# Performance work log

Hardware: AMD Instinct MI355X
Metric: run time of the kernel (lower is better)

## Reference

```python
import jax, jax.numpy as jnp
import numpy as np

B, S, E, H = 2, 2048, 2048, 16
D = E // H

def setup_inputs() -> dict:
    key = jax.random.key(0)
    ks = jax.random.split(key, 9)
    sc = 1.0 / np.sqrt(E)
    return {
        "x":  jax.random.normal(ks[0], (B, S, E), jnp.float32),
        "Wq": jax.random.normal(ks[1], (E, E), jnp.float32) * sc,
        "bq": jax.random.normal(ks[2], (E,), jnp.float32) * 0.01,
        "Wk": jax.random.normal(ks[3], (E, E), jnp.float32) * sc,
        "bk": jax.random.normal(ks[4], (E,), jnp.float32) * 0.01,
        "Wv": jax.random.normal(ks[5], (E, E), jnp.float32) * sc,
        "bv": jax.random.normal(ks[6], (E,), jnp.float32) * 0.01,
        "Wo": jax.random.normal(ks[7], (E, E), jnp.float32) * sc,
        "bo": jax.random.normal(ks[8], (E,), jnp.float32) * 0.01,
    }

def _split_heads(t):
    # [B,S,E] -> [B,H,S,D]
    return t.reshape(B, S, H, D).transpose(0, 2, 1, 3)

def reference(x, Wq, bq, Wk, bk, Wv, bv, Wo, bo):
    # projections (nn.Linear: y = x @ W^T + b)
    q = _split_heads(x @ Wq.T + bq)
    k = _split_heads(x @ Wk.T + bk)
    v = _split_heads(x @ Wv.T + bv)

    # scaled causal attention; scale uses k.size(-1) == head_dim D
    scores = jnp.einsum("bhqd,bhkd->bhqk", q, k) / jnp.sqrt(jnp.asarray(D, q.dtype))
    causal = jnp.tril(jnp.ones((S, S), bool))  # [S,S]
    scores = jnp.where(causal[None, None, :, :], scores, -jnp.inf)
    # training path subtracts row max before softmax (no-op under stable softmax)
    scores = scores - jnp.max(scores, axis=-1, keepdims=True)
    attn = jax.nn.softmax(scores, axis=-1)
    # dropout_rate = 0.0 -> identity
    ctx = jnp.einsum("bhqk,bhkd->bhqd", attn, v)

    # merge heads [B,H,S,D] -> [B,S,E], final projection
    out = ctx.transpose(0, 2, 1, 3).reshape(B, S, E)
    return out @ Wo.T + bo
```

## Files before the change

### kernel.cpp

```cpp
#include <hip/hip_runtime.h>

typedef unsigned short u16;
typedef __attribute__((ext_vector_type(4))) float f32x4;
typedef __attribute__((ext_vector_type(8))) short s16x8;
typedef __attribute__((ext_vector_type(4))) unsigned short u16x4;
typedef __attribute__((ext_vector_type(2))) unsigned u32x2;

#define MFMA16(a, b, c) __builtin_amdgcn_mfma_f32_16x16x32_bf16((a), (b), (c), 0, 0, 0)

__device__ __forceinline__ u16 f2bf(float f) {
  union { float f; unsigned u; } v; v.f = f;
  unsigned u = v.u;
  u += 0x7fffu + ((u >> 16) & 1u);
  return (u16)(u >> 16);
}

__device__ __forceinline__ unsigned cvtpk(float a, float b) {
  unsigned r;
  asm("v_cvt_pk_bf16_f32 %0, %1, %2" : "=v"(r) : "v"(a), "v"(b));
  return r;
}

__device__ __forceinline__ void gl_lds16(const void* g, void* l) {
  __builtin_amdgcn_global_load_lds(
      (const __attribute__((address_space(1))) void*)g,
      (__attribute__((address_space(3))) void*)l, 16, 0, 0);
}

#define BARF()                                  \
  asm volatile("" ::: "memory");                \
  __builtin_amdgcn_s_barrier();                 \
  asm volatile("" ::: "memory")

__global__ void cast6(const float* __restrict__ x,
                      const float* __restrict__ w0, const float* __restrict__ w1,
                      const float* __restrict__ w2, const float* __restrict__ w3,
                      u16* __restrict__ ws) {
  const int y = blockIdx.y;
  const float* src;
  u16* dst;
  if (y < 2) { src = x + (size_t)y * 4194304; dst = ws + (size_t)y * 4194304; }
  else {
    src = (y == 2) ? w0 : (y == 3) ? w1 : (y == 4) ? w2 : w3;
    dst = ws + 8388608 + (size_t)(y - 2) * 4194304;
  }
  const int i = blockIdx.x * 256 + threadIdx.x;
  f32x4 v = ((const f32x4*)src)[i];
  u16x4 o;
#pragma unroll
  for (int e = 0; e < 4; ++e) o[e] = f2bf(v[e]);
  ((u16x4*)dst)[i] = o;
}

__global__ __launch_bounds__(512, 2) void gemm_qk256(
    const u16* __restrict__ A,
    const u16* __restrict__ W0, const u16* __restrict__ W1,
    const float* __restrict__ b0, const float* __restrict__ b1,
    u16* __restrict__ Qo, u16* __restrict__ Ko) {
  __shared__ __align__(16) u16 smem[65536];
  const int z = blockIdx.z;
  const u16* Bw = z ? W1 : W0;
  const float* bias = z ? b1 : b0;
  u16* out = z ? Ko : Qo;
  const float scale = z ? 1.0f : 0.1275174306003988f;

  const int tid = threadIdx.x;
  const int lane = tid & 63, w = tid >> 6;
  const int ln = lane & 15, quad = lane >> 4, ln7 = lane & 7;
  const int m0 = blockIdx.y * 256, n0 = blockIdx.x * 256;
  const int wm = (w >> 2) << 7, wn = (w & 3) << 6;

  const int r0 = tid >> 3;
  const int ck = ((tid & 7) ^ (r0 & 7)) << 3;
  const int abase = wm * 64;
  const int bbase = 16384 + wn * 64;
  const int sw0 = (quad ^ ln7) << 3, sw1 = ((4 + quad) ^ ln7) << 3;

  f32x4 acc[8][4] = {};
  s16x8 af[8][2], bf[4][2];

  auto STGA = [&](int t) {
    u16* dst = smem + ((t & 1) << 15);
    const int kc = t << 6;
    const u16* s0 = A + (size_t)(m0 + r0) * 2048 + kc + ck;
#pragma unroll
    for (int g = 0; g < 4; ++g)
      gl_lds16(s0 + (size_t)(g * 64) * 2048, dst + g * 4096 + tid * 8);
  };
  auto STGB = [&](int t) {
    u16* dst = smem + ((t & 1) << 15) + 16384;
    const int kc = t << 6;
    const u16* s0 = Bw + (size_t)(n0 + r0) * 2048 + kc + ck;
#pragma unroll
    for (int g = 0; g < 4; ++g)
      gl_lds16(s0 + (size_t)(g * 64) * 2048, dst + g * 4096 + tid * 8);
  };
  auto RDA = [&](int buf, int tm0) {
    const u16* p = smem + (buf << 15) + abase;
#pragma unroll
    for (int u = 0; u < 4; ++u) {
      const int tt = tm0 + u;
      af[tt][0] = *(const s16x8*)&p[(tt * 16 + ln) * 64 + sw0];
      af[tt][1] = *(const s16x8*)&p[(tt * 16 + ln) * 64 + sw1];
    }
  };
  auto RDB = [&](int buf, int tn0) {
    const u16* p = smem + (buf << 15) + bbase;
#pragma unroll
    for (int u = 0; u < 2; ++u) {
      const int tt = tn0 + u;
      bf[tt][0] = *(const s16x8*)&p[(tt * 16 + ln) * 64 + sw0];
      bf[tt][1] = *(const s16x8*)&p[(tt * 16 + ln) * 64 + sw1];
    }
  };
  auto QM = [&](int tm0, int tn0) {
    __builtin_amdgcn_s_setprio(1);
#pragma unroll
    for (int tm = tm0; tm < tm0 + 4; ++tm)
#pragma unroll
      for (int tn = tn0; tn < tn0 + 2; ++tn)
#pragma unroll
        for (int ks = 0; ks < 2; ++ks)
          acc[tm][tn] = MFMA16(bf[tn][ks], af[tm][ks], acc[tm][tn]);
    __builtin_amdgcn_s_setprio(0);
  };

  STGA(0); STGB(0);
#pragma unroll 1
  for (int t = 0; t < 32; ++t) {
    const int cb = t & 1;
    asm volatile("s_waitcnt vmcnt(0)" ::: "memory");
    BARF();
    if (t < 31) { STGA(t + 1); STGB(t + 1); }
    RDA(cb, 0); RDB(cb, 0);
    QM(0, 0);
    RDA(cb, 4);
    QM(4, 0);
    RDB(cb, 2);
    QM(4, 2);
    QM(0, 2);
  }
  asm volatile("s_waitcnt vmcnt(0) lgkmcnt(0)" ::: "memory");

#pragma unroll
  for (int tn = 0; tn < 4; ++tn) {
    const int n_base = n0 + wn + tn * 16 + quad * 4;
    const f32x4 bv = *(const f32x4*)&bias[n_base];
    const int h = n_base >> 7, dl = n_base & 127;
#pragma unroll
    for (int tm = 0; tm < 8; ++tm) {
      const int m = m0 + wm + tm * 16 + ln;
      const int b = m >> 11, s = m & 2047;
      u16x4 ov;
#pragma unroll
      for (int r = 0; r < 4; ++r) ov[r] = f2bf((acc[tm][tn][r] + bv[r]) * scale);
      *(u16x4*)&out[(((size_t)(b * 16 + h)) << 18) + ((size_t)s << 7) + dl] = ov;
    }
  }
}

template <int SWAP>
__device__ __forceinline__ void gemm1b_n128(const u16* __restrict__ A,
                                            const u16* __restrict__ Bw,
                                            u16* smem, f32x4 (&acc)[4][4],
                                            int m0, int n0, int tid) {
  const int lane = tid & 63, w = tid >> 6;
  const int ln = lane & 15, quad = lane >> 4, ln7 = lane & 7;
  const int wm = (w >> 1) * 64, wn = (w & 1) * 64;
  const int r0 = tid >> 3;
  const int ck = ((tid & 7) ^ (r0 & 7)) << 3;
  const int sw0 = (quad ^ ln7) << 3, sw1 = ((4 + quad) ^ ln7) << 3;

  s16x8 af[4][2], bf[4][2];

  auto STG = [&](int t) {
    u16* dst = smem + (t & 1) * 24576;
    const int kc = t << 6;
    const u16* sa = A + (size_t)(m0 + r0) * 2048 + kc + ck;
#pragma unroll
    for (int g = 0; g < 4; ++g)
      gl_lds16(sa + (size_t)(g * 64) * 2048, dst + g * 4096 + tid * 8);
    const u16* sb = Bw + (size_t)(n0 + r0) * 2048 + kc + ck;
#pragma unroll
    for (int g = 0; g < 2; ++g)
      gl_lds16(sb + (size_t)(g * 64) * 2048, dst + 16384 + g * 4096 + tid * 8);
  };
  auto RD = [&](int buf) {
    const u16* pa = smem + buf * 24576 + wm * 64;
    const u16* pb = smem + buf * 24576 + 16384 + wn * 64;
#pragma unroll
    for (int tt = 0; tt < 4; ++tt) {
      af[tt][0] = *(const s16x8*)&pa[(tt * 16 + ln) * 64 + sw0];
      af[tt][1] = *(const s16x8*)&pa[(tt * 16 + ln) * 64 + sw1];
      bf[tt][0] = *(const s16x8*)&pb[(tt * 16 + ln) * 64 + sw0];
      bf[tt][1] = *(const s16x8*)&pb[(tt * 16 + ln) * 64 + sw1];
    }
  };

  STG(0);
#pragma unroll 1
  for (int t = 0; t < 32; ++t) {
    asm volatile("s_waitcnt vmcnt(0)" ::: "memory");
    BARF();
    if (t < 31) STG(t + 1);
    RD(t & 1);
    __builtin_amdgcn_s_setprio(1);
#pragma unroll
    for (int tm = 0; tm < 4; ++tm)
#pragma unroll
      for (int tn = 0; tn < 4; ++tn)
#pragma unroll
        for (int ks = 0; ks < 2; ++ks)
          acc[tm][tn] = SWAP ? MFMA16(bf[tn][ks], af[tm][ks], acc[tm][tn])
                             : MFMA16(af[tm][ks], bf[tn][ks], acc[tm][tn]);
    __builtin_amdgcn_s_setprio(0);
  }
  asm volatile("s_waitcnt vmcnt(0) lgkmcnt(0)" ::: "memory");
}

__global__ __launch_bounds__(512, 2) void gemm_v(const u16* __restrict__ A,
                                                 const u16* __restrict__ Bw,
                                                 const float* __restrict__ bias,
                                                 u16* __restrict__ Vo) {
  __shared__ __align__(16) u16 smem[49152];
  const int tid = threadIdx.x;
  const int lane = tid & 63, w = tid >> 6;
  const int ln = lane & 15, quad = lane >> 4;
  const int m0 = blockIdx.y * 256, n0 = blockIdx.x * 128;
  const int wm = (w >> 1) * 64, wn = (w & 1) * 64;

  f32x4 acc[4][4] = {};
  gemm1b_n128<0>(A, Bw, smem, acc, m0, n0, tid);
  const int b = m0 >> 11;
#pragma unroll
  for (int tn = 0; tn < 4; ++tn) {
    const int n = n0 + wn + tn * 16 + ln;
    const float bv = bias[n];
    const int h = n >> 7, dl = n & 127;
#pragma unroll
    for (int tm = 0; tm < 4; ++tm) {
      const int s_base = (m0 & 2047) + wm + tm * 16 + quad * 4;
      u16x4 ov;
#pragma unroll
      for (int r = 0; r < 4; ++r) ov[r] = f2bf(acc[tm][tn][r] + bv);
      *(u16x4*)&Vo[(((size_t)((b * 16 + h) * 128 + dl)) << 11) + s_base] = ov;
    }
  }
}

__global__ __launch_bounds__(512, 2) void gemm_out(const u16* __restrict__ A,
                                                   const u16* __restrict__ Bw,
                                                   const float* __restrict__ bias,
                                                   float* __restrict__ out) {
  __shared__ __align__(16) u16 smem[49152];
  const int tid = threadIdx.x;
  const int lane = tid & 63, w = tid >> 6;
  const int ln = lane & 15, quad = lane >> 4;
  const int m0 = blockIdx.y * 256, n0 = blockIdx.x * 128;
  const int wm = (w >> 1) * 64, wn = (w & 1) * 64;

  f32x4 acc[4][4] = {};
  gemm1b_n128<1>(A, Bw, smem, acc, m0, n0, tid);
#pragma unroll
  for (int tn = 0; tn < 4; ++tn) {
    const int n_base = n0 + wn + tn * 16 + quad * 4;
    const f32x4 bv = *(const f32x4*)&bias[n_base];
#pragma unroll
    for (int tm = 0; tm < 4; ++tm) {
      const int m = m0 + wm + tm * 16 + ln;
      f32x4 ov;
#pragma unroll
      for (int r = 0; r < 4; ++r) ov[r] = acc[tm][tn][r] + bv[r];
      *(f32x4*)&out[(size_t)m * 2048 + n_base] = ov;
    }
  }
}

__global__ __launch_bounds__(256, 2) void attn_kernel(const u16* __restrict__ Q,
                                                      const u16* __restrict__ Kp,
                                                      const u16* __restrict__ Vt,
                                                      u16* __restrict__ ctx) {
  __shared__ __align__(16) u16 smem[40960];
  u16* sP = smem;

  const int flat = blockIdx.x + (blockIdx.y << 4);
  const int bh = flat >> 4;
  const int i = (flat < 256) ? (15 - (flat & 15)) : (flat & 15);
  const size_t base = (size_t)bh << 18;

  const int tid = threadIdx.x, lane = tid & 63, w = tid >> 6;
  const int ln = lane & 15, quad = lane >> 4, ln7 = lane & 7;

#pragma unroll
  for (int c = 0; c < 8; ++c) {
    const int chunk0 = (c * 4 + w) * 64;
    const int chunk = chunk0 + lane;
    const int row = chunk >> 4, cc = chunk & 15;
    gl_lds16(Q + base + (size_t)((i * 128 + row) * 128 + ((cc ^ (row & 15)) << 3)),
             (char*)(smem + 8192) + chunk0 * 16);
  }
  __syncthreads();
  s16x8 qf[2][4];
#pragma unroll
  for (int qt = 0; qt < 2; ++qt)
#pragma unroll
    for (int kc = 0; kc < 4; ++kc)
      qf[qt][kc] = *(const s16x8*)&smem[8192 + (w * 32 + qt * 16 + ln) * 128 +
                                        (((kc * 4 + quad) ^ ln) << 3)];
  __syncthreads();

  auto stageK = [&](int j, int buf) {
    u16* dst = smem + 8192 + buf * 8192;
#pragma unroll
    for (int c = 0; c < 4; ++c) {
      const int chunk0 = (c * 4 + w) * 64;
      const int chunk = chunk0 + lane;
      const int row = chunk >> 4, cc = chunk & 15;
      gl_lds16(Kp + base + (size_t)((j * 64 + row) * 128 + ((cc ^ (row & 15)) << 3)),
               (char*)dst + chunk0 * 16);
    }
  };
  auto stageV = [&](int j, int buf) {
    u16* dst = smem + 24576 + buf * 8192;
#pragma unroll
    for (int c = 0; c < 4; ++c) {
      const int chunk0 = (c * 4 + w) * 64;
      const int chunk = chunk0 + lane;
      const int row = chunk >> 3, cc = chunk & 7;
      gl_lds16(Vt + base + (size_t)(row * 2048 + j * 64 + ((cc ^ (row & 7)) << 3)),
               (char*)dst + chunk0 * 16);
    }
  };

  stageK(0, 0);
  stageV(0, 0);
  __syncthreads();

  f32x4 o_acc[8][2] = {};
  float lsum[2] = {0.f, 0.f};
  const int jmax = 2 * i + 1;
  const int qg = i * 128 + w * 32 + ln;

  for (int j = 0; j <= jmax; ++j) {
    const int cb = j & 1;
    if (j < jmax) { stageK(j + 1, cb ^ 1); stageV(j + 1, cb ^ 1); }
    const u16* sK = smem + 8192 + cb * 8192;
    const u16* sV = smem + 24576 + cb * 8192;

    f32x4 sacc[4][2] = {};
#pragma unroll
    for (int kc = 0; kc < 4; ++kc) {
      s16x8 kf[4];
#pragma unroll
      for (int kt = 0; kt < 4; ++kt)
        kf[kt] = *(const s16x8*)&sK[(kt * 16 + ln) * 128 + (((kc * 4 + quad) ^ ln) << 3)];
#pragma unroll
      for (int kt = 0; kt < 4; ++kt)
#pragma unroll
        for (int qt = 0; qt < 2; ++qt)
          sacc[kt][qt] = MFMA16(kf[kt], qf[qt][kc], sacc[kt][qt]);
    }

    const bool diag = (j >= 2 * i);
#pragma unroll
    for (int kt = 0; kt < 4; ++kt)
#pragma unroll
      for (int qt = 0; qt < 2; ++qt) {
        f32x4 pv;
#pragma unroll
        for (int r = 0; r < 4; ++r) {
          float p = __builtin_amdgcn_exp2f(sacc[kt][qt][r]);
          const int kg = j * 64 + kt * 16 + quad * 4 + r;
          if (diag && kg > qg + qt * 16) p = 0.f;
          lsum[qt] += p;
          pv[r] = p;
        }
        u32x2 pk2;
        pk2[0] = cvtpk(pv[0], pv[1]);
        pk2[1] = cvtpk(pv[2], pv[3]);
        const int qrow = w * 32 + qt * 16 + ln;
        const int c = kt * 4 + quad;
        *(u32x2*)&sP[qrow * 64 + ((c ^ (qrow & 14)) << 2)] = pk2;
      }
    asm volatile("s_waitcnt lgkmcnt(0)" ::: "memory");
    __builtin_amdgcn_sched_barrier(0);

#pragma unroll
    for (int kc = 0; kc < 2; ++kc) {
      s16x8 vf[8], pf[2];
#pragma unroll
      for (int qt = 0; qt < 2; ++qt) {
        const int qrow = w * 32 + qt * 16 + ln;
        const int c0 = kc * 8 + quad * 2;
        pf[qt] = *(const s16x8*)&sP[qrow * 64 + ((c0 ^ (qrow & 14)) << 2)];
      }
#pragma unroll
      for (int dt = 0; dt < 8; ++dt)
        vf[dt] = *(const s16x8*)&sV[(dt * 16 + ln) * 64 + (((kc * 4 + quad) ^ ln7) << 3)];
#pragma unroll
      for (int dt = 0; dt < 8; ++dt)
#pragma unroll
        for (int qt = 0; qt < 2; ++qt)
          o_acc[dt][qt] = MFMA16(vf[dt], pf[qt], o_acc[dt][qt]);
    }
    __syncthreads();
  }

  const int b = bh >> 4, h = bh & 15;
  float rinv[2];
#pragma unroll
  for (int qt = 0; qt < 2; ++qt) {
    float s = lsum[qt];
    s += __shfl_xor(s, 16);
    s += __shfl_xor(s, 32);
    rinv[qt] = __builtin_amdgcn_rcpf(s);
  }
#pragma unroll
  for (int dt = 0; dt < 8; ++dt)
#pragma unroll
    for (int qt = 0; qt < 2; ++qt) {
      const int sg = i * 128 + w * 32 + qt * 16 + ln;
      const int d0 = h * 128 + dt * 16 + quad * 4;
      u16x4 ov;
#pragma unroll
      for (int r = 0; r < 4; ++r) ov[r] = f2bf(o_acc[dt][qt][r] * rinv[qt]);
      *(u16x4*)&ctx[((size_t)b << 22) + (size_t)sg * 2048 + d0] = ov;
    }
}

extern "C" void kernel_launch(void* const* d_in, const int* in_sizes, int n_in,
                              void* d_out, int out_size, void* d_ws, size_t ws_size,
                              hipStream_t stream) {
  const float* x = (const float*)d_in[0];
  const float* Wq = (const float*)d_in[1];
  const float* bq = (const float*)d_in[2];
  const float* Wk = (const float*)d_in[3];
  const float* bk = (const float*)d_in[4];
  const float* Wv = (const float*)d_in[5];
  const float* bv = (const float*)d_in[6];
  const float* Wo = (const float*)d_in[7];
  const float* bo = (const float*)d_in[8];

  u16* ws = (u16*)d_ws;
  u16* xb = ws;
  u16* Wqb = xb + 8388608;
  u16* Wkb = Wqb + 4194304;
  u16* Wvb = Wkb + 4194304;
  u16* Wob = Wvb + 4194304;
  u16* Qb = Wob + 4194304;
  u16* Kb = Qb + 8388608;
  u16* Vtb = Kb + 8388608;
  u16* ctxb = Vtb + 8388608;

  cast6<<<dim3(4096, 6), 256, 0, stream>>>(x, Wq, Wk, Wv, Wo, ws);

  gemm_qk256<<<dim3(8, 16, 2), 512, 0, stream>>>(xb, Wqb, Wkb, bq, bk, Qb, Kb);
  gemm_v<<<dim3(16, 16), 512, 0, stream>>>(xb, Wvb, bv, Vtb);

  attn_kernel<<<dim3(16, 32), 256, 0, stream>>>(Qb, Kb, Vtb, ctxb);

  gemm_out<<<dim3(16, 16), 512, 0, stream>>>(ctxb, Wob, bo, (float*)d_out);
}
```

Baseline: 339.9 us.

## Restructure GEMM pipelines with split-phase staging and a triple-buffered K loop

The QK projection GEMM now stages A and B tiles in separate phases interleaved with MFMA groups, using a row-blocked smem layout and prefetching one stage ahead with partial waitcnt, instead of a single wait-then-load per iteration. The V and output GEMMs move to a three-buffer ring with K split into two half-steps, so loads for step t+2 overlap compute on step t. The aim is to hide global-to-LDS latency behind MFMA work. In exchange, LDS use per block rises to 144KB for the n128 GEMMs, which may lower occupancy, and there are more barriers per iteration.

```diff
diff --git a/kernel.cpp b/kernel.cpp
--- a/kernel.cpp
+++ b/kernel.cpp
@@ -70,10 +70,11 @@
   const int m0 = blockIdx.y * 256, n0 = blockIdx.x * 256;
   const int wm = (w >> 2) << 7, wn = (w & 3) << 6;
 
-  const int r0 = tid >> 3;
-  const int ck = ((tid & 7) ^ (r0 & 7)) << 3;
-  const int abase = wm * 64;
-  const int bbase = 16384 + wn * 64;
+  const int ci0 = tid, ci1 = 512 + tid;
+  const int r0 = ci0 >> 3, c0k = ((ci0 & 7) ^ (r0 & 7)) << 3;
+  const int r1 = ci1 >> 3, c1k = ((ci1 & 7) ^ (r1 & 7)) << 3;
+  const int abase = (w >> 2) << 13;
+  const int bbase = 16384 + (((w >> 1) & 1) << 13) + ((w & 1) << 12);
   const int sw0 = (quad ^ ln7) << 3, sw1 = ((4 + quad) ^ ln7) << 3;
 
   f32x4 acc[8][4] = {};
@@ -81,19 +82,23 @@
 
   auto STGA = [&](int t) {
     u16* dst = smem + ((t & 1) << 15);
-    const int kc = t << 6;
-    const u16* s0 = A + (size_t)(m0 + r0) * 2048 + kc + ck;
-#pragma unroll
-    for (int g = 0; g < 4; ++g)
-      gl_lds16(s0 + (size_t)(g * 64) * 2048, dst + g * 4096 + tid * 8);
+    const int kc = (t & 31) << 6;
+    const u16* s0 = A + (size_t)(m0 + r0) * 2048 + kc + c0k;
+    const u16* s1 = A + (size_t)(m0 + r1) * 2048 + kc + c1k;
+    gl_lds16(s0, dst + ci0 * 8);
+    gl_lds16(s1, dst + ci1 * 8);
+    gl_lds16(s0 + (size_t)128 * 2048, dst + 8192 + ci0 * 8);
+    gl_lds16(s1 + (size_t)128 * 2048, dst + 8192 + ci1 * 8);
   };
   auto STGB = [&](int t) {
     u16* dst = smem + ((t & 1) << 15) + 16384;
-    const int kc = t << 6;
-    const u16* s0 = Bw + (size_t)(n0 + r0) * 2048 + kc + ck;
-#pragma unroll
-    for (int g = 0; g < 4; ++g)
-      gl_lds16(s0 + (size_t)(g * 64) * 2048, dst + g * 4096 + tid * 8);
+    const int kc = (t & 31) << 6;
+    const u16* s0 = Bw + (size_t)(n0 + r0) * 2048 + kc + c0k;
+    const u16* s1 = Bw + (size_t)(n0 + r1) * 2048 + kc + c1k;
+    gl_lds16(s0, dst + ci0 * 8);
+    gl_lds16(s1, dst + ci1 * 8);
+    gl_lds16(s0 + (size_t)128 * 2048, dst + 8192 + ci0 * 8);
+    gl_lds16(s1 + (size_t)128 * 2048, dst + 8192 + ci1 * 8);
   };
   auto RDA = [&](int buf, int tm0) {
     const u16* p = smem + (buf << 15) + abase;
@@ -125,20 +130,42 @@
     __builtin_amdgcn_s_setprio(0);
   };
 
-  STGA(0); STGB(0);
+  STGA(0); STGB(0); STGA(1);
+  asm volatile("s_waitcnt vmcnt(4)" ::: "memory");
+  BARF();
+  RDA(0, 0); RDB(0, 0);
+
 #pragma unroll 1
-  for (int t = 0; t < 32; ++t) {
-    const int cb = t & 1;
+  for (int u = 0; u < 16; ++u) {
+    const int t = 2 * u;
+    QM(0, 0);
+    RDA(0, 4);
+    STGB(t + 1);
+    BARF();
+    QM(4, 0);
+    RDB(0, 2);
+    BARF();
+    QM(4, 2);
     asm volatile("s_waitcnt vmcnt(0)" ::: "memory");
     BARF();
-    if (t < 31) { STGA(t + 1); STGB(t + 1); }
-    RDA(cb, 0); RDB(cb, 0);
+    QM(0, 2);
+    RDA(1, 0); RDB(1, 0);
+    STGA(t + 2);
+    BARF();
     QM(0, 0);
-    RDA(cb, 4);
+    RDA(1, 4);
+    STGB(t + 2);
+    BARF();
     QM(4, 0);
-    RDB(cb, 2);
+    RDB(1, 2);
+    BARF();
     QM(4, 2);
+    asm volatile("s_waitcnt vmcnt(0)" ::: "memory");
+    BARF();
     QM(0, 2);
+    RDA(0, 0); RDB(0, 0);
+    STGA(t + 3);
+    BARF();
   }
   asm volatile("s_waitcnt vmcnt(0) lgkmcnt(0)" ::: "memory");
 
@@ -160,7 +187,7 @@
 }
 
 template <int SWAP>
-__device__ __forceinline__ void gemm1b_n128(const u16* __restrict__ A,
+__device__ __forceinline__ void gemm3r_n128(const u16* __restrict__ A,
                                             const u16* __restrict__ Bw,
                                             u16* smem, f32x4 (&acc)[4][4],
                                             int m0, int n0, int tid) {
@@ -173,8 +200,8 @@
 
   s16x8 af[4][2], bf[4][2];
 
-  auto STG = [&](int t) {
-    u16* dst = smem + (t & 1) * 24576;
+  auto STG = [&](int t, int buf) {
+    u16* dst = smem + buf * 24576;
     const int kc = t << 6;
     const u16* sa = A + (size_t)(m0 + r0) * 2048 + kc + ck;
 #pragma unroll
@@ -185,35 +212,65 @@
     for (int g = 0; g < 2; ++g)
       gl_lds16(sb + (size_t)(g * 64) * 2048, dst + 16384 + g * 4096 + tid * 8);
   };
-  auto RD = [&](int buf) {
+  auto RD0 = [&](int buf) {
     const u16* pa = smem + buf * 24576 + wm * 64;
     const u16* pb = smem + buf * 24576 + 16384 + wn * 64;
 #pragma unroll
     for (int tt = 0; tt < 4; ++tt) {
       af[tt][0] = *(const s16x8*)&pa[(tt * 16 + ln) * 64 + sw0];
+      bf[tt][0] = *(const s16x8*)&pb[(tt * 16 + ln) * 64 + sw0];
+    }
+  };
+  auto RD1 = [&](int buf) {
+    const u16* pa = smem + buf * 24576 + wm * 64;
+    const u16* pb = smem + buf * 24576 + 16384 + wn * 64;
+#pragma unroll
+    for (int tt = 0; tt < 4; ++tt) {
       af[tt][1] = *(const s16x8*)&pa[(tt * 16 + ln) * 64 + sw1];
-      bf[tt][0] = *(const s16x8*)&pb[(tt * 16 + ln) * 64 + sw0];
       bf[tt][1] = *(const s16x8*)&pb[(tt * 16 + ln) * 64 + sw1];
     }
   };
-
-  STG(0);
+  auto QM0 = [&]() {
+    __builtin_amdgcn_s_setprio(1);
+#pragma unroll
+    for (int tm = 0; tm < 4; ++tm)
+#pragma unroll
+      for (int tn = 0; tn < 4; ++tn)
+        acc[tm][tn] = SWAP ? MFMA16(bf[tn][0], af[tm][0], acc[tm][tn])
+                           : MFMA16(af[tm][0], bf[tn][0], acc[tm][tn]);
+    __builtin_amdgcn_s_setprio(0);
+  };
+  auto QM1 = [&]() {
+    __builtin_amdgcn_s_setprio(1);
+#pragma unroll
+    for (int tm = 0; tm < 4; ++tm)
+#pragma unroll
+      for (int tn = 0; tn < 4; ++tn)
+        acc[tm][tn] = SWAP ? MFMA16(bf[tn][1], af[tm][1], acc[tm][tn])
+                           : MFMA16(af[tm][1], bf[tn][1], acc[tm][tn]);
+    __builtin_amdgcn_s_setprio(0);
+  };
+
+  STG(0, 0); STG(1, 1);
+  asm volatile("s_waitcnt vmcnt(6)" ::: "memory");
+  BARF();
+  RD0(0);
+
+  int bc = 0;
 #pragma unroll 1
   for (int t = 0; t < 32; ++t) {
-    asm volatile("s_waitcnt vmcnt(0)" ::: "memory");
-    BARF();
-    if (t < 31) STG(t + 1);
-    RD(t & 1);
-    __builtin_amdgcn_s_setprio(1);
-#pragma unroll
-    for (int tm = 0; tm < 4; ++tm)
-#pragma unroll
-      for (int tn = 0; tn < 4; ++tn)
-#pragma unroll
-        for (int ks = 0; ks < 2; ++ks)
-          acc[tm][tn] = SWAP ? MFMA16(bf[tn][ks], af[tm][ks], acc[tm][tn])
-                             : MFMA16(af[tm][ks], bf[tn][ks], acc[tm][tn]);
-    __builtin_amdgcn_s_setprio(0);
+    const int bn = (bc == 2) ? 0 : bc + 1;
+    const int bs = (bn == 2) ? 0 : bn + 1;
+    QM0();
+    RD1(bc);
+    if (t < 30) STG(t + 2, bs);
+    BARF();
+    QM1();
+    if (t < 30) { asm volatile("s_waitcnt vmcnt(6)" ::: "memory"); }
+    else        { asm volatile("s_waitcnt vmcnt(0)" ::: "memory"); }
+    BARF();
+    if (t < 31) RD0(bn);
+    bc = bn;
   }
   asm volatile("s_waitcnt vmcnt(0) lgkmcnt(0)" ::: "memory");
 }
@@ -222,7 +279,7 @@
                                                  const u16* __restrict__ Bw,
                                                  const float* __restrict__ bias,
                                                  u16* __restrict__ Vo) {
-  __shared__ __align__(16) u16 smem[49152];
+  __shared__ __align__(16) u16 smem[73728];
   const int tid = threadIdx.x;
   const int lane = tid & 63, w = tid >> 6;
   const int ln = lane & 15, quad = lane >> 4;
@@ -230,7 +287,7 @@
   const int wm = (w >> 1) * 64, wn = (w & 1) * 64;
 
   f32x4 acc[4][4] = {};
-  gemm1b_n128<0>(A, Bw, smem, acc, m0, n0, tid);
+  gemm3r_n128<0>(A, Bw, smem, acc, m0, n0, tid);
   const int b = m0 >> 11;
 #pragma unroll
   for (int tn = 0; tn < 4; ++tn) {
@@ -252,7 +309,7 @@
                                                    const u16* __restrict__ Bw,
                                                    const float* __restrict__ bias,
                                                    float* __restrict__ out) {
-  __shared__ __align__(16) u16 smem[49152];
+  __shared__ __align__(16) u16 smem[73728];
   const int tid = threadIdx.x;
   const int lane = tid & 63, w = tid >> 6;
   const int ln = lane & 15, quad = lane >> 4;
@@ -260,7 +317,7 @@
   const int wm = (w >> 1) * 64, wn = (w & 1) * 64;
 
   f32x4 acc[4][4] = {};
-  gemm1b_n128<1>(A, Bw, smem, acc, m0, n0, tid);
+  gemm3r_n128<1>(A, Bw, smem, acc, m0, n0, tid);
 #pragma unroll
   for (int tn = 0; tn < 4; ++tn) {
     const int n_base = n0 + wn + tn * 16 + quad * 4;
```

Result: no change. 333.7 us (-1.8%).
